# Kernel tuning notes

Measured on AMD Instinct MI355X. Metric: run time of the kernel, lower is better.

The kernel has to match this reference:

```python
import jax, jax.numpy as jnp
import numpy as np
from collections import deque

SIGMA_LOW = 0.02  # TreeFilter2D(sigma=0.02); high-level trees use sigma=1 (low_tree=False)


def bilinear_resize(x, oh, ow):
    # torch F.interpolate(mode='bilinear', align_corners=False)
    B, C, H, W = x.shape
    sy, sx = H / oh, W / ow
    ys = jnp.maximum((jnp.arange(oh, dtype=jnp.float32) + 0.5) * sy - 0.5, 0.0)
    xs = jnp.maximum((jnp.arange(ow, dtype=jnp.float32) + 0.5) * sx - 0.5, 0.0)
    y0 = jnp.clip(jnp.floor(ys).astype(jnp.int32), 0, H - 1)
    x0 = jnp.clip(jnp.floor(xs).astype(jnp.int32), 0, W - 1)
    y1 = jnp.minimum(y0 + 1, H - 1)
    x1 = jnp.minimum(x0 + 1, W - 1)
    wy = (ys - y0).reshape(oh, 1)
    wx = (xs - x0).reshape(1, ow)
    top, bot = x[:, :, y0, :], x[:, :, y1, :]
    v00, v01 = top[:, :, :, x0], top[:, :, :, x1]
    v10, v11 = bot[:, :, :, x0], bot[:, :, :, x1]
    return ((1 - wy) * (1 - wx)) * v00 + ((1 - wy) * wx) * v01 + (wy * (1 - wx)) * v10 + (wy * wx) * v11


def nearest_resize(x, oh, ow):
    B, C, H, W = x.shape
    yi = jnp.minimum((jnp.arange(oh) * (H / oh)).astype(jnp.int32), H - 1)
    xi = jnp.minimum((jnp.arange(ow) * (W / ow)).astype(jnp.int32), W - 1)
    return x[:, :, yi, :][:, :, :, xi]


def _mst_adj(feat, h, w):
    # Kruskal MST on 4-connected grid; edge weight = norm2_distance of features.
    n = h * w
    idx = np.arange(n).reshape(h, w)
    eu = np.concatenate([idx[:, :-1].ravel(), idx[:-1, :].ravel()])
    ev = np.concatenate([idx[:, 1:].ravel(), idx[1:, :].ravel()])
    f = feat.reshape(feat.shape[0], -1).astype(np.float64)
    d = ((f[:, eu] - f[:, ev]) ** 2).sum(axis=0)
    order = np.argsort(d, kind='stable')
    pa = np.arange(n)

    def find(a):
        r = a
        while pa[r] != r:
            r = pa[r]
        while pa[a] != r:
            pa[a], a = r, pa[a]
        return r

    adj = [[] for _ in range(n)]
    cnt = 0
    for e in order:
        u, v = int(eu[e]), int(ev[e])
        ru, rv = find(u), find(v)
        if ru != rv:
            pa[ru] = rv
            adj[u].append(v)
            adj[v].append(u)
            cnt += 1
            if cnt == n - 1:
                break
    return adj


def build_forest(embed):
    # embed: np [B,C,h,w] -> global parent array (ids b*n+i) + per-BFS-level node lists
    B, C, h, w = embed.shape
    n = h * w
    parent = np.arange(B * n)
    level = np.zeros(B * n, dtype=np.int64)
    for b in range(B):
        adj = _mst_adj(embed[b], h, w)
        lv = np.full(n, -1, dtype=np.int64)
        lv[0] = 0
        q = deque([0])
        while q:
            u = q.popleft()
            for v in adj[u]:
                if lv[v] < 0:
                    lv[v] = lv[u] + 1
                    parent[b * n + v] = b * n + u
                    q.append(v)
        level[b * n:(b + 1) * n] = lv
    d = int(level.max())
    levels = [np.nonzero(level == l)[0] for l in range(1, d + 1)]
    return jnp.asarray(parent), levels


def tree_filter(feature, embed, parent, levels, sigma):
    # feature [B,C,n], embed [B,Ce,n]; normalized tree filtering:
    # y_i = sum_j prod(path-edge-weights) x_j / sum_j prod(path-edge-weights)
    B, C, n = feature.shape
    ones = jnp.ones((B, 1, n), feature.dtype)
    xg = jnp.moveaxis(jnp.concatenate([feature, ones], axis=1), 0, 1).reshape(C + 1, B * n)
    eg = jnp.moveaxis(embed, 0, 1).reshape(embed.shape[1], B * n)
    wgt = jnp.exp(-((eg - eg[:, parent]) ** 2).sum(axis=0) / sigma)  # [B*n]; root entries unused
    # upward (leaf->root) subtree aggregation
    A = xg
    for idx in reversed(levels):
        A = A.at[:, parent[idx]].add(wgt[idx] * A[:, idx])
    # downward (root->leaf) completion
    F = A
    for idx in levels:
        F = F.at[:, idx].set(A[:, idx] + wgt[idx] * (F[:, parent[idx]] - wgt[idx] * A[:, idx]))
    y = F[:C] / F[C]
    return jnp.moveaxis(y.reshape(C, B, n), 0, 1)  # [B,C,n]


def setup_inputs() -> dict:
    key = jax.random.key(0)
    ks = jax.random.split(key, 6)
    B, K, h, w = 8, 4, 48, 48
    C = 512
    preds = jax.random.normal(ks[0], (B, K, h, w), jnp.float32)
    low_feats = jax.random.uniform(ks[1], (B, 3, 192, 192), jnp.float32) * 0.1
    hf1 = jax.random.normal(ks[2], (B, C, 24, 24), jnp.float32) * 0.05
    hf2 = jax.random.normal(ks[3], (B, C, 12, 12), jnp.float32) * 0.05
    hf3 = jax.random.normal(ks[4], (B, C, 6, 6), jnp.float32) * 0.05
    rois = (jax.random.uniform(ks[5], (B, 192, 192)) > 0.5).astype(jnp.float32)
    weight = jnp.asarray(0.4, jnp.float32)
    return {"preds": preds, "low_feats": low_feats, "high_feats_1": hf1,
            "high_feats_2": hf2, "high_feats_3": hf3, "unlabeled_ROIs": rois,
            "weight": weight}


def reference(preds, low_feats, high_feats_1, high_feats_2, high_feats_3, unlabeled_ROIs, weight):
    B, K, h, w = preds.shape
    low = bilinear_resize(low_feats, h, w)                     # no_grad in original
    roi = nearest_resize(unlabeled_ROIs[:, None], h, w)        # [B,1,h,w]
    N = roi.sum()
    prob = jax.nn.softmax(preds, axis=1)
    probf = prob.reshape(B, K, -1)
    roif = roi.reshape(B, 1, -1)

    parent0, lv0 = build_forest(np.asarray(low))
    AS = tree_filter(probf, low.reshape(B, low.shape[1], -1), parent0, lv0, SIGMA_LOW)

    loss = jnp.zeros((), preds.dtype)
    for hf in (high_feats_1, high_feats_2, high_feats_3):
        hfi = bilinear_resize(hf, h, w)
        p, lv = build_forest(np.asarray(hfi))
        AS_k = tree_filter(AS, hfi.reshape(B, hfi.shape[1], -1), p, lv, 1.0)
        loss = loss + (roif * jnp.abs(probf - AS_k)).sum()
    loss = jnp.where(N > 0, loss / N, loss)
    return weight * loss
```

## Files before the change

### kernel.cpp

```cpp
#include <hip/hip_runtime.h>
#include <math.h>


#define HH 48
#define WW 48
#define NN (HH*WW)
#define EHH (HH*(WW-1))
#define EEE (2*EHH)
#define BB 8
#define KK 4
#define TPB 256
#define TPE 512
#define TPW 1024
#define TPF 512
#define NPL 5
#define NPN 5
#define ESLOT (4*NN)
#define LVE (2*(NN-1))
#define RIPT ((LVE+TPW-1)/TPW)
#define SENTN 0xFFFFu
#define MAXT 12

#define SSTRIDE_W (4*NN+8)
#define PK_OFF 0
#define D_OFF (4*NN)

__device__ __forceinline__ void edge_uv(int e,int& u,int& v){
  if(e<EHH){ int r=e/(WW-1); int c=e-r*(WW-1); u=r*WW+c; v=u+1; }
  else     { int t=e-EHH; u=t; v=t+WW; }
}

__device__ __forceinline__ void pick_src(int f, const float* lowf, const float* hf1,
                                         const float* hf2, const float* hf3,
                                         const float*& src, int& sh, int& C){
  if(f==0){src=lowf; sh=192; C=3;}
  else if(f==1){src=hf1; sh=24; C=512;}
  else if(f==2){src=hf2; sh=12; C=512;}
  else        {src=hf3; sh=6;  C=512;}
}

__global__ __launch_bounds__(TPB) void k_prob(const float* __restrict__ preds,
                                              float* __restrict__ probf){
  int t=blockIdx.x*TPB+threadIdx.x;
  if(t>=BB*NN) return;
  int b=t/NN, i=t-b*NN;
  const float* p=preds+(size_t)b*KK*NN+i;
  float x0=p[0],x1=p[NN],x2=p[2*NN],x3=p[3*NN];
  float mx=fmaxf(fmaxf(x0,x1),fmaxf(x2,x3));
  float e0=expf(x0-mx),e1=expf(x1-mx),e2=expf(x2-mx),e3=expf(x3-mx);
  float s=((e0+e1)+(e2+e3));
  float* q=probf+(size_t)b*KK*NN+i;
  q[0]=e0/s; q[NN]=e1/s; q[2*NN]=e2/s; q[3*NN]=e3/s;
}

__global__ __launch_bounds__(TPE) void k_edges(
  const float* __restrict__ lowf, const float* __restrict__ hf1,
  const float* __restrict__ hf2, const float* __restrict__ hf3,
  double* __restrict__ pd_low, double* __restrict__ pd_hf, int nchunk)
{
  __shared__ float up[4*NN+64];
  __shared__ int   y0t[48], y1t[48];
  __shared__ float wyt[48];
  const int tid=threadIdx.x;
  int pidx, chunk, hfidx=0;
  if(blockIdx.x<8){ pidx=blockIdx.x; chunk=0; }
  else { int t=blockIdx.x-8; hfidx=t/nchunk; chunk=t-hfidx*nchunk; pidx=8+hfidx; }
  const int f=pidx>>3, b=pidx&7;
  const float* src; int sh,C;
  pick_src(f,lowf,hf1,hf2,hf3,src,sh,C);
  const int shw=sh*sh;
  const float* srcb=src+(size_t)b*C*shw;
  const int cpc=(f==0)?3:(512/nchunk);
  const int c_begin=chunk*cpc;
  const int c_end=(c_begin+cpc<C)?(c_begin+cpc):C;

  if(tid<48){
    float sy=(float)sh/48.0f;
    float ys=fmaxf(((float)tid+0.5f)*sy-0.5f,0.0f);
    int y0=(int)ys; if(y0>sh-1) y0=sh-1;
    int y1=y0+1; if(y1>sh-1) y1=sh-1;
    y0t[tid]=y0; y1t[tid]=y1; wyt[tid]=ys-(float)y0;
  }

  double accH[NPN], accV[NPN];
  #pragma unroll
  for(int j=0;j<NPN;j++){ accH[j]=0.0; accV[j]=0.0; }

  for(int c0=c_begin;c0<c_end;c0+=4){
    const int nc=(c_end-c0<4)?(c_end-c0):4;
    __syncthreads();
    for(int i=tid;i<NN;i+=TPE){
      int r=i/WW, c=i-r*WW;
      int y0=y0t[r], y1=y1t[r]; float wy=wyt[r];
      int x0=y0t[c], x1=y1t[c]; float wx=wyt[c];
      float w00=(1.0f-wy)*(1.0f-wx), w01=(1.0f-wy)*wx;
      float w10=wy*(1.0f-wx),        w11=wy*wx;
      int o00=y0*sh+x0, o01=y0*sh+x1, o10=y1*sh+x0, o11=y1*sh+x1;
      const float* pl=srcb+(size_t)c0*shw;
      for(int cc=0;cc<nc;cc++){
        const float* p=pl+(size_t)cc*shw;
        up[cc*NN+i]=w00*p[o00]+w01*p[o01]+w10*p[o10]+w11*p[o11];
      }
    }
    __syncthreads();
    #pragma unroll
    for(int j=0;j<NPN;j++){
      int u=tid+j*TPE;
      if(u<NN){
        int r=u/WW, c=u-r*WW;
        bool hOK=(c<WW-1), vOK=(r<HH-1);
        for(int cc=0;cc<nc;cc++){
          const float* pu=up+cc*NN+u;
          float a=pu[0], b1=pu[1], c1=pu[WW];
          if(hOK){ double d=(double)a-(double)b1; accH[j]=fma(d,d,accH[j]); }
          if(vOK){ double d=(double)a-(double)c1; accV[j]=fma(d,d,accV[j]); }
        }
      }
    }
  }
  double* outp=(f==0)? pd_low+(size_t)pidx*EEE
                     : pd_hf+((size_t)hfidx*nchunk+chunk)*EEE;
  #pragma unroll
  for(int j=0;j<NPN;j++){
    int u=tid+j*TPE;
    if(u<NN){
      int r=u/WW, c=u-r*WW;
      if(c<WW-1) outp[r*(WW-1)+c]=accH[j];
      if(r<HH-1) outp[EHH+u]=accV[j];
    }
  }
}

__global__ __launch_bounds__(TPB) void k_redux(
  const double* __restrict__ pd_low, const double* __restrict__ pd_hf,
  int nchunk, double* __restrict__ dkeyG)
{
  int t=blockIdx.x*TPB+threadIdx.x;
  if(t>=32*EEE) return;
  int pidx=t/EEE, e=t-pidx*EEE;
  double s;
  if(pidx<8) s=pd_low[(size_t)pidx*EEE+e];
  else {
    const double* p0=pd_hf+((size_t)(pidx-8)*nchunk)*EEE+e;
    s=0.0;
    for(int k=0;k<nchunk;k++) s+=p0[(size_t)k*EEE];
  }
  dkeyG[t]=s;
}

__global__ __launch_bounds__(TPW) void k_struct(
  const double* __restrict__ dkeyG, int* __restrict__ sbase,
  int* __restrict__ ancT, float* __restrict__ prodT)
{
  __shared__ __align__(16) char smem[123600];
  double*             dkey =(double*)(smem+0);
  unsigned char*      mstf =(unsigned char*)(smem+36096);
  unsigned long long* bestd=(unsigned long long*)(smem+40608);
  int*                comp =(int*)(smem+59040);
  int*                beste=(int*)(smem+68256);
  int*                lnk  =(int*)(smem+77472);
  float4*             adjw =(float4*)(smem+40608);
  unsigned char*      adjS =(unsigned char*)(smem+77472);
  int*                chunkS=(int*)(smem+79776);
  unsigned int*       eA   =(unsigned int*)(smem+0);
  unsigned int*       eB   =(unsigned int*)(smem+86688);
  int*                flags=(int*)(smem+123552);
  int*                ancA =(int*)(smem+0);
  float*              prmA =(float*)(smem+9216);
  int*                ancB =(int*)(smem+18432);
  float*              prmB =(float*)(smem+27648);

  const int tid=threadIdx.x;
  const int pidx=blockIdx.x;
  const int f=pidx>>3;
  const float sigma=(f==0)?0.02f:1.0f;

  {
    const double* p0=dkeyG+(size_t)pidx*EEE;
    for(int e=tid;e<EEE;e+=TPW) dkey[e]=p0[e];
    for(int i=tid;i<NN;i+=TPW) comp[i]=i;
    for(int e=tid;e<EEE;e+=TPW) mstf[e]=0;
    __syncthreads();

    for(int round=0;round<20;++round){
      for(int i=tid;i<NN;i+=TPW){ bestd[i]=~0ull; beste[i]=0x7fffffff; lnk[i]=i; }
      if(tid==0) flags[1]=0;
      __syncthreads();
      for(int e=tid;e<EEE;e+=TPW){
        int u,v; edge_uv(e,u,v);
        int cu=comp[u], cv=comp[v];
        if(cu!=cv){
          unsigned long long db=(unsigned long long)__double_as_longlong(dkey[e]);
          atomicMin(&bestd[cu],db);
          atomicMin(&bestd[cv],db);
        }
      }
      __syncthreads();
      for(int e=tid;e<EEE;e+=TPW){
        int u,v; edge_uv(e,u,v);
        int cu=comp[u], cv=comp[v];
        if(cu!=cv){
          unsigned long long db=(unsigned long long)__double_as_longlong(dkey[e]);
          if(db==bestd[cu]) atomicMin(&beste[cu],e);
          if(db==bestd[cv]) atomicMin(&beste[cv],e);
        }
      }
      __syncthreads();
      for(int i=tid;i<NN;i+=TPW){
        if(comp[i]==i && beste[i]!=0x7fffffff){
          int e=beste[i]; int u,v; edge_uv(e,u,v);
          int cu=comp[u], cv=comp[v];
          int other=(cu==i)?cv:cu;
          bool mutual=(beste[other]==e);
          if(!mutual || other<i){ lnk[i]=other; mstf[e]=1; flags[1]=1; }
        }
      }
      __syncthreads();
      if(flags[1]==0) break;
      {
        volatile int* vl=lnk;
        for(int i=tid;i<NN;i+=TPW){
          int x=comp[i];
          int p=vl[x];
          int gp=vl[p];
          while(p!=gp){
            vl[x]=gp;
            x=p; p=gp; gp=vl[p];
          }
          comp[i]=p;
        }
      }
      __syncthreads();
    }
    __syncthreads();

    for(int i=tid;i<NN;i+=TPW){
      int r=i/WW, c=i-r*WW;
      int mask=0; float4 w; w.x=0.0f; w.y=0.0f; w.z=0.0f; w.w=0.0f;
      if(c>0    && mstf[r*(WW-1)+c-1]){ mask|=1; w.x=expf(-(float)dkey[r*(WW-1)+c-1]/sigma); }
      if(c<WW-1 && mstf[r*(WW-1)+c])  { mask|=2; w.y=expf(-(float)dkey[r*(WW-1)+c]/sigma); }
      if(r>0    && mstf[EHH+i-WW])    { mask|=4; w.z=expf(-(float)dkey[EHH+i-WW]/sigma); }
      if(r<HH-1 && mstf[EHH+i])       { mask|=8; w.w=expf(-(float)dkey[EHH+i]/sigma); }
      adjw[i]=w;
      adjS[i]=(unsigned char)mask;
    }
    if(tid==0) flags[2]=0;
    __syncthreads();
  }

  {
    const int m0=adjS[0];
    const int d0=(m0&1)?0:((m0&2)?1:((m0&4)?2:3));
    const int e0=d0;

    for(int t=tid;t<ESLOT;t+=TPW){
      int u=t>>2, d=t&3;
      unsigned int pk=0;
      if(adjS[u]&(1<<d)){
        int v=(d==0)?u-1:(d==1)?u+1:(d==2)?u-WW:u+WW;
        int rd=d^1;
        int mv=adjS[v];
        int nd=rd;
        #pragma unroll
        for(int k2=4;k2>=1;k2--){ int dd=(rd+k2)&3; if(mv&(1<<dd)) nd=dd; }
        int ne=(v<<2)|nd;
        unsigned int nxt=(ne==e0)?SENTN:(unsigned int)ne;
        pk=(nxt<<16)|1u;
      }
      eA[t]=pk;
    }
    __syncthreads();

    unsigned int* P=eA; unsigned int* Q=eB;
    for(int r2=0;r2<13;r2++){
      for(int t=tid;t<ESLOT;t+=TPW){
        unsigned int pk=P[t];
        unsigned int dist=pk&0xFFFFu, nxt=pk>>16;
        if(dist && nxt!=SENTN){
          unsigned int pk2=P[nxt];
          dist+=pk2&0xFFFFu;
          nxt=pk2>>16;
          pk=(nxt<<16)|dist;
        }
        Q[t]=pk;
      }
      __syncthreads();
      unsigned int* tmp=P; P=Q; Q=tmp;
    }
    for(int t=tid;t<ESLOT;t+=TPW){
      unsigned int dist=P[t]&0xFFFFu;
      Q[t]=dist?(unsigned int)(LVE-(int)dist):0xFFFFFFFFu;
    }
    __syncthreads();

    int* scanA=(int*)P;
    for(int t=tid;t<ESLOT;t+=TPW){
      unsigned int pos=Q[t];
      if(pos!=0xFFFFFFFFu){
        int u=t>>2, d=t&3;
        int v=(d==0)?u-1:(d==1)?u+1:(d==2)?u-WW:u+WW;
        unsigned int rpos=Q[(v<<2)|(d^1)];
        scanA[pos]=(pos<rpos)?1:-1;
      }
    }
    __syncthreads();

    const int base=tid*RIPT;
    int vals[RIPT]; int lsum=0;
    #pragma unroll
    for(int j=0;j<RIPT;j++){
      int p=base+j;
      int v=(p<LVE)?scanA[p]:0;
      lsum+=v; vals[j]=lsum;
    }
    chunkS[tid]=lsum;
    __syncthreads();
    for(int off=1;off<TPW;off<<=1){
      int v=chunkS[tid];
      int vv=(tid>=off)?chunkS[tid-off]:0;
      __syncthreads();
      chunkS[tid]=v+vv;
      __syncthreads();
    }
    const int myoff=(tid>0)?chunkS[tid-1]:0;
    int mymax=0;
    #pragma unroll
    for(int j=0;j<RIPT;j++){
      int p=base+j;
      if(p<LVE){ int s=vals[j]+myoff; scanA[p]=s; if(s>mymax) mymax=s; }
    }
    if(mymax>0) atomicMax(&flags[2],mymax);
    __syncthreads();

    int* sp=sbase+(size_t)pidx*SSTRIDE_W;
    int4* g_pk=(int4*)(sp+PK_OFF);
    if(tid==0){
      g_pk[0]=make_int4(0,__float_as_int(0.0f),0,0);
      sp[D_OFF]=flags[2];
    }
    for(int t=tid;t<ESLOT;t+=TPW){
      unsigned int pos=Q[t];
      if(pos!=0xFFFFFFFFu){
        int u=t>>2, d=t&3;
        int v=(d==0)?u-1:(d==1)?u+1:(d==2)?u-WW:u+WW;
        unsigned int rpos=Q[(v<<2)|(d^1)];
        if(pos<rpos){
          float4 w4=adjw[u];
          float w=(d==0)?w4.x:(d==1)?w4.y:(d==2)?w4.z:w4.w;
          g_pk[v]=make_int4(u,__float_as_int(w),scanA[pos],0);
        }
      }
    }
    __syncthreads();
  }

  {
    const int* sp=sbase+(size_t)pidx*SSTRIDE_W;
    const int4* g_pk=(const int4*)(sp+PK_OFF);
    const int maxD=flags[2];
    int T=1; while((1<<T)<=maxD) T++;
    int* gA=ancT+(size_t)pidx*MAXT*NN;
    float* gP=prodT+(size_t)pidx*MAXT*NN;
    int* aP=ancA; int* aQ=ancB; float* pP=prmA; float* pQ=prmB;
    for(int i=tid;i<NN;i+=TPW){
      int4 rec=g_pk[i];
      aP[i]=rec.x; pP[i]=__int_as_float(rec.y);
      gA[i]=rec.x; gP[i]=pP[i];
    }
    __syncthreads();
    for(int t=1;t<T;t++){
      for(int i=tid;i<NN;i+=TPW){
        int a=aP[i];
        int a2=aP[a]; float pr=pP[i]*pP[a];
        aQ[i]=a2; pQ[i]=pr;
        gA[(size_t)t*NN+i]=a2; gP[(size_t)t*NN+i]=pr;
      }
      __syncthreads();
      { int* t1=aP; aP=aQ; aQ=t1; float* t2=pP; pP=pQ; pQ=t2; }
    }
  }
}

__global__ __launch_bounds__(TPF) void k_fchan(
  const float* __restrict__ X, float* __restrict__ Fout,
  const int* __restrict__ sbase, const int* __restrict__ ancT,
  const float* __restrict__ prodT, int pidx0)
{
  __shared__ float S[NN];
  __shared__ float Sb[NN];
  const int tid=threadIdx.x;
  const int pg=blockIdx.x/5, c=blockIdx.x%5;
  const int pidx=pidx0+pg;
  const int xb=pg&7;
  const int* sp=sbase+(size_t)pidx*SSTRIDE_W;
  const int4* g_pk=(const int4*)(sp+PK_OFF);
  const int maxD=sp[D_OFF];
  int T=1; while((1<<T)<=maxD) T++;
  const int* ancP=ancT+(size_t)pidx*MAXT*NN;
  const float* prmP=prodT+(size_t)pidx*MAXT*NN;

  int dep[NPL]; float wv[NPL];
  #pragma unroll
  for(int j=0;j<NPL;j++){
    int i=tid+j*TPF;
    if(i<NN){
      int4 rec=g_pk[i];
      dep[j]=rec.z; wv[j]=__int_as_float(rec.y);
      S[i]=(c<4)? X[((size_t)xb*KK+c)*NN+i] : 1.0f;
    } else { dep[j]=-1; wv[j]=0.0f; }
  }
  __syncthreads();

  for(int t=0;t<T;t++){
    float sn[NPL]; int aj[NPL]; float pj[NPL];
    #pragma unroll
    for(int j=0;j<NPL;j++){
      int i=tid+j*TPF;
      if(i<NN){ sn[j]=S[i]; aj[j]=ancP[(size_t)t*NN+i]; pj[j]=prmP[(size_t)t*NN+i]; }
      else { sn[j]=0.0f; aj[j]=0; pj[j]=0.0f; }
    }
    __syncthreads();
    int bit=1<<t;
    #pragma unroll
    for(int j=0;j<NPL;j++){
      if(dep[j]>=bit) atomicAdd(&S[aj[j]], pj[j]*sn[j]);
    }
    __syncthreads();
  }

  #pragma unroll
  for(int j=0;j<NPL;j++){
    int i=tid+j*TPF;
    if(i<NN){ float fq=1.0f-wv[j]*wv[j]; Sb[i]=fq*S[i]; }
  }
  __syncthreads();

  float* Sp=Sb; float* Sq=S;
  for(int t=0;t<T;t++){
    float bn[NPL];
    #pragma unroll
    for(int j=0;j<NPL;j++){
      int i=tid+j*TPF;
      if(i<NN){
        int a=ancP[(size_t)t*NN+i]; float ai=prmP[(size_t)t*NN+i];
        bn[j]=fmaf(ai,Sp[a],Sp[i]);
      } else bn[j]=0.0f;
    }
    __syncthreads();
    #pragma unroll
    for(int j=0;j<NPL;j++){
      int i=tid+j*TPF;
      if(i<NN) Sq[i]=bn[j];
    }
    __syncthreads();
    { float* tmp=Sp; Sp=Sq; Sq=tmp; }
  }
  float* o=Fout+(size_t)blockIdx.x*NN;
  for(int i=tid;i<NN;i+=TPF) o[i]=Sp[i];
}

__global__ __launch_bounds__(TPB) void k_div0(const float* __restrict__ FA,
                                              float* __restrict__ AS){
  int t=blockIdx.x*TPB+threadIdx.x;
  if(t>=BB*KK*NN) return;
  int b=t/(KK*NN), rem=t-b*(KK*NN), c=rem/NN, i=rem-c*NN;
  float inv=1.0f/FA[((size_t)b*5+4)*NN+i];
  AS[t]=FA[((size_t)b*5+c)*NN+i]*inv;
}

__global__ __launch_bounds__(TPB) void k_loss(
  const float* __restrict__ FB, const float* __restrict__ probf,
  const float* __restrict__ rois, float* __restrict__ partials)
{
  __shared__ float red[TPB];
  const int tid=threadIdx.x;
  const int fb=blockIdx.x;
  const int b=fb&7;
  const float* pb=probf+(size_t)b*KK*NN;
  float part=0.0f;
  for(int i=tid;i<NN;i+=TPB){
    int r=i/WW, c2=i-r*WW;
    float roi=rois[(size_t)b*(192*192)+(4*r)*192+(4*c2)];
    float inv=1.0f/FB[((size_t)fb*5+4)*NN+i];
    float s=fabsf(pb[i]      -FB[((size_t)fb*5+0)*NN+i]*inv)
          + fabsf(pb[NN+i]   -FB[((size_t)fb*5+1)*NN+i]*inv)
          + fabsf(pb[2*NN+i] -FB[((size_t)fb*5+2)*NN+i]*inv)
          + fabsf(pb[3*NN+i] -FB[((size_t)fb*5+3)*NN+i]*inv);
    part+=roi*s;
  }
  red[tid]=part; __syncthreads();
  for(int s2=TPB/2;s2>0;s2>>=1){ if(tid<s2) red[tid]+=red[tid+s2]; __syncthreads(); }
  if(tid==0) partials[fb]=red[0];
}

__global__ __launch_bounds__(TPB) void k_final(const float* __restrict__ rois,
    const float* __restrict__ partials, const float* __restrict__ wt,
    float* __restrict__ out)
{
  __shared__ float red[TPB];
  const int tid=threadIdx.x;
  float n=0.0f;
  for(int t=tid;t<BB*NN;t+=TPB){
    int b=t/NN, i=t-b*NN; int r=i/WW, c=i-r*WW;
    n += rois[(size_t)b*(192*192)+(4*r)*192+(4*c)];
  }
  red[tid]=n; __syncthreads();
  for(int s=TPB/2;s>0;s>>=1){ if(tid<s) red[tid]+=red[tid+s]; __syncthreads(); }
  if(tid==0){
    float loss=0.0f;
    for(int j=0;j<3*BB;j++) loss+=partials[j];
    float N=red[0];
    out[0]=wt[0]*((N>0.0f)?(loss/N):loss);
  }
}

extern "C" void kernel_launch(void* const* d_in, const int* in_sizes, int n_in,
                              void* d_out, int out_size, void* d_ws, size_t ws_size,
                              hipStream_t stream) {
  (void)in_sizes; (void)n_in; (void)out_size;
  const float* preds=(const float*)d_in[0];
  const float* lowf =(const float*)d_in[1];
  const float* hf1  =(const float*)d_in[2];
  const float* hf2  =(const float*)d_in[3];
  const float* hf3  =(const float*)d_in[4];
  const float* rois =(const float*)d_in[5];
  const float* wt   =(const float*)d_in[6];
  float* out=(float*)d_out;

  char* ws=(char*)d_ws;
  float* partials=(float*)ws;
  float* probf=(float*)(ws+256);
  float* AS   =(float*)(ws+256+(size_t)BB*KK*NN*4);
  size_t sb_off=256+(size_t)2*BB*KK*NN*4;
  int*   sbase=(int*)(ws+sb_off);
  size_t dk_off=sb_off+(size_t)32*SSTRIDE_W*4;
  double* dkeyG=(double*)(ws+dk_off);
  size_t pl_off=dk_off+(size_t)32*EEE*8;
  double* pd_low=(double*)(ws+pl_off);
  size_t ph_off=pl_off+(size_t)8*EEE*8;
  double* pd_hf=(double*)(ws+ph_off);

  int*   ancT =(int*)  (ws+ph_off);
  float* prodT=(float*)(ws+ph_off+(size_t)32*MAXT*NN*4);
  float* FA   =(float*)(ws+ph_off+(size_t)2*32*MAXT*NN*4);
  float* FB   =(float*)(ws+ph_off+(size_t)2*32*MAXT*NN*4+(size_t)40*NN*4);

  int nchunk=32;
  if(ph_off+(size_t)24*32*EEE*8>ws_size) nchunk=16;

  k_prob<<<(BB*NN+TPB-1)/TPB,TPB,0,stream>>>(preds,probf);
  k_edges<<<8+24*nchunk,TPE,0,stream>>>(lowf,hf1,hf2,hf3,pd_low,pd_hf,nchunk);
  k_redux<<<(32*EEE+TPB-1)/TPB,TPB,0,stream>>>(pd_low,pd_hf,nchunk,dkeyG);
  k_struct<<<32,TPW,0,stream>>>(dkeyG,sbase,ancT,prodT);
  k_fchan<<<40,TPF,0,stream>>>(probf,FA,sbase,ancT,prodT,0);
  k_div0<<<(BB*KK*NN+TPB-1)/TPB,TPB,0,stream>>>(FA,AS);
  k_fchan<<<120,TPF,0,stream>>>(AS,FB,sbase,ancT,prodT,8);
  k_loss<<<3*BB,TPB,0,stream>>>(FB,probf,rois,partials);
  k_final<<<1,TPB,0,stream>>>(rois,partials,wt,out);
}
```

Measured before the change: 227.0 us.

## Fuse softmax into edge kernel, trim Boruvka barriers, use wave-shuffle scan

The softmax kernel is folded into k_edges as extra trailing blocks, which removes one kernel launch. In the Boruvka MST loop, the reset of bestd/beste/flags moves to the end of the previous round, so each round needs one fewer __syncthreads. The block-wide prefix scan over 1024 threads changes from a barrier-heavy Hillis-Steele scan in LDS to a two-level wave shuffle scan. These mainly cut launch and barrier overhead. The added work is more shared-state ordering to reason about, and the lnk reset within a round now relies on later barriers.

```diff
diff --git a/kernel.cpp b/kernel.cpp
--- a/kernel.cpp
+++ b/kernel.cpp
@@ -39,29 +39,33 @@
   else        {src=hf3; sh=6;  C=512;}
 }
 
-__global__ __launch_bounds__(TPB) void k_prob(const float* __restrict__ preds,
-                                              float* __restrict__ probf){
-  int t=blockIdx.x*TPB+threadIdx.x;
-  if(t>=BB*NN) return;
-  int b=t/NN, i=t-b*NN;
-  const float* p=preds+(size_t)b*KK*NN+i;
-  float x0=p[0],x1=p[NN],x2=p[2*NN],x3=p[3*NN];
-  float mx=fmaxf(fmaxf(x0,x1),fmaxf(x2,x3));
-  float e0=expf(x0-mx),e1=expf(x1-mx),e2=expf(x2-mx),e3=expf(x3-mx);
-  float s=((e0+e1)+(e2+e3));
-  float* q=probf+(size_t)b*KK*NN+i;
-  q[0]=e0/s; q[NN]=e1/s; q[2*NN]=e2/s; q[3*NN]=e3/s;
-}
-
 __global__ __launch_bounds__(TPE) void k_edges(
   const float* __restrict__ lowf, const float* __restrict__ hf1,
   const float* __restrict__ hf2, const float* __restrict__ hf3,
+  const float* __restrict__ preds, float* __restrict__ probf,
   double* __restrict__ pd_low, double* __restrict__ pd_hf, int nchunk)
 {
   __shared__ float up[4*NN+64];
   __shared__ int   y0t[48], y1t[48];
   __shared__ float wyt[48];
   const int tid=threadIdx.x;
+  const int nEB=8+24*nchunk;
+
+  if(blockIdx.x>=nEB){
+    int t=(blockIdx.x-nEB)*TPE+tid;
+    if(t<BB*NN){
+      int b=t/NN, i=t-b*NN;
+      const float* p=preds+(size_t)b*KK*NN+i;
+      float x0=p[0],x1=p[NN],x2=p[2*NN],x3=p[3*NN];
+      float mx=fmaxf(fmaxf(x0,x1),fmaxf(x2,x3));
+      float e0=expf(x0-mx),e1=expf(x1-mx),e2=expf(x2-mx),e3=expf(x3-mx);
+      float s=((e0+e1)+(e2+e3));
+      float* q=probf+(size_t)b*KK*NN+i;
+      q[0]=e0/s; q[NN]=e1/s; q[2*NN]=e2/s; q[3*NN]=e3/s;
+    }
+    return;
+  }
+
   int pidx, chunk, hfidx=0;
   if(blockIdx.x<8){ pidx=blockIdx.x; chunk=0; }
   else { int t=blockIdx.x-8; hfidx=t/nchunk; chunk=t-hfidx*nchunk; pidx=8+hfidx; }
@@ -180,12 +184,12 @@
     for(int e=tid;e<EEE;e+=TPW) dkey[e]=p0[e];
     for(int i=tid;i<NN;i+=TPW) comp[i]=i;
     for(int e=tid;e<EEE;e+=TPW) mstf[e]=0;
+    for(int i=tid;i<NN;i+=TPW){ bestd[i]=~0ull; beste[i]=0x7fffffff; lnk[i]=i; }
+    if(tid==0) flags[1]=0;
     __syncthreads();
 
     for(int round=0;round<20;++round){
-      for(int i=tid;i<NN;i+=TPW){ bestd[i]=~0ull; beste[i]=0x7fffffff; lnk[i]=i; }
-      if(tid==0) flags[1]=0;
-      __syncthreads();
+      for(int i=tid;i<NN;i+=TPW) lnk[i]=i;
       for(int e=tid;e<EEE;e+=TPW){
         int u,v; edge_uv(e,u,v);
         int cu=comp[u], cv=comp[v];
@@ -230,6 +234,8 @@
           comp[i]=p;
         }
       }
+      for(int i=tid;i<NN;i+=TPW){ bestd[i]=~0ull; beste[i]=0x7fffffff; }
+      if(tid==0) flags[1]=0;
       __syncthreads();
     }
     __syncthreads();
@@ -313,16 +319,27 @@
       int v=(p<LVE)?scanA[p]:0;
       lsum+=v; vals[j]=lsum;
     }
-    chunkS[tid]=lsum;
-    __syncthreads();
-    for(int off=1;off<TPW;off<<=1){
-      int v=chunkS[tid];
-      int vv=(tid>=off)?chunkS[tid-off]:0;
-      __syncthreads();
-      chunkS[tid]=v+vv;
-      __syncthreads();
-    }
-    const int myoff=(tid>0)?chunkS[tid-1]:0;
+    const int lane=tid&63, wid=tid>>6;
+    int x=lsum;
+    #pragma unroll
+    for(int off=1;off<64;off<<=1){
+      int y=__shfl_up(x,off,64);
+      if(lane>=off) x+=y;
+    }
+    if(lane==63) chunkS[wid]=x;
+    __syncthreads();
+    if(wid==0 && lane<16){
+      int w=chunkS[lane];
+      #pragma unroll
+      for(int off=1;off<16;off<<=1){
+        int y=__shfl_up(w,off,64);
+        if(lane>=off) w+=y;
+      }
+      chunkS[lane]=w;
+    }
+    __syncthreads();
+    const int waveoff=(wid>0)?chunkS[wid-1]:0;
+    const int myoff=x+waveoff-lsum;
     int mymax=0;
     #pragma unroll
     for(int j=0;j<RIPT;j++){
@@ -548,8 +565,9 @@
   int nchunk=32;
   if(ph_off+(size_t)24*32*EEE*8>ws_size) nchunk=16;
 
-  k_prob<<<(BB*NN+TPB-1)/TPB,TPB,0,stream>>>(preds,probf);
-  k_edges<<<8+24*nchunk,TPE,0,stream>>>(lowf,hf1,hf2,hf3,pd_low,pd_hf,nchunk);
+  const int nEB=8+24*nchunk;
+  const int nSM=(BB*NN+TPE-1)/TPE;
+  k_edges<<<nEB+nSM,TPE,0,stream>>>(lowf,hf1,hf2,hf3,preds,probf,pd_low,pd_hf,nchunk);
   k_redux<<<(32*EEE+TPB-1)/TPB,TPB,0,stream>>>(pd_low,pd_hf,nchunk,dkeyG);
   k_struct<<<32,TPW,0,stream>>>(dkeyG,sbase,ancT,prodT);
   k_fchan<<<40,TPF,0,stream>>>(probf,FA,sbase,ancT,prodT,0);
```

Result: faster. 221.4 us (-2.4%).
